# Kernel optimization log

Measured on AMD Instinct MI355X. Metric: run time of the kernel, lower is better.

## Reference

```python
import jax, jax.numpy as jnp
import numpy as np

NUM_GROUPS = 128
GROUP_SIZE = 1024
N_POINTS = 262144


def setup_inputs() -> dict:
    key = jax.random.key(0)
    k1, k2, k3, k4 = jax.random.split(key, 4)
    point_cloud = jax.random.normal(k1, (1, 3, N_POINTS), dtype=jnp.float32)
    # pointwise-MLP feature extractor params (3 -> 64 -> 128 -> 1024)
    w1 = jax.random.normal(k2, (3, 64), dtype=jnp.float32) * 0.1
    w2 = jax.random.normal(k3, (64, 128), dtype=jnp.float32) * 0.1
    w3 = jax.random.normal(k4, (128, 1024), dtype=jnp.float32) * 0.03
    return {"point_cloud": point_cloud, "w1": w1, "w2": w2, "w3": w3}


def _fps(points, num_groups):
    # points: [N, 3]. Seed = point farthest from the centroid (as in source),
    # then iterative farthest-point sampling. The source recomputes distances
    # to every sampled point each step; keeping a running min-distance is
    # mathematically identical.
    centroid = points.mean(axis=0, keepdims=True)
    d0 = jnp.linalg.norm(points - centroid, axis=1)  # [N]
    first = jnp.argmax(d0)
    min_dist = jnp.linalg.norm(points - points[first], axis=1)  # [N]

    def step(min_dist, _):
        nxt = jnp.argmax(min_dist)
        d = jnp.linalg.norm(points - points[nxt], axis=1)
        return jnp.minimum(min_dist, d), nxt

    _, idx_rest = jax.lax.scan(step, min_dist, None, length=num_groups - 1)
    return jnp.concatenate([first[None], idx_rest])  # [G]


def reference(point_cloud, w1, w2, w3):
    pc = point_cloud[0].T  # [N, 3]  (squeeze(0).permute(1,0))
    fps_idx = _fps(pc, NUM_GROUPS)
    sampled = pc[fps_idx]  # [G, 3]
    # Brute-force KNN (sklearn kneighbors equivalent): squared dists [G, N]
    d2 = (jnp.sum(sampled * sampled, axis=1, keepdims=True)
          - 2.0 * (sampled @ pc.T)
          + jnp.sum(pc * pc, axis=1)[None, :])
    _, knn_idx = jax.lax.top_k(-d2, GROUP_SIZE)  # [G, K] nearest indices
    groups = pc[knn_idx]  # [G, K, 3] irregular gather
    # feature_: per-point MLP + max-pool over the K points of each patch.
    # (Pointwise op => batching all G groups at once equals the source's
    # pairwise batched calls.)
    h = jax.nn.relu(groups @ w1)       # [G, K, 64]
    h = jax.nn.relu(h @ w2)            # [G, K, 128]
    h = h @ w3                         # [G, K, 1024]
    patch_features = h.max(axis=1)     # [G, 1024]
    return patch_features, sampled
```

## Files before the change

### kernel.cpp

```cpp
#include <hip/hip_runtime.h>

#define N_PTS 262144
#define NG 128
#define GS 1024
#define FPS_B 16

typedef __attribute__((ext_vector_type(8))) short short8;
typedef __attribute__((ext_vector_type(8))) __bf16 bf16x8;
typedef __attribute__((ext_vector_type(4))) float f32x4;
typedef unsigned long long ull;

__device__ __forceinline__ unsigned short f2bf(float f) {
  unsigned u = __float_as_uint(f);
  unsigned r = u + 0x7FFFu + ((u >> 16) & 1u);
  return (unsigned short)(r >> 16);
}

__device__ __forceinline__ f32x4 mfma16(short8 a, short8 b, f32x4 c) {
  return __builtin_amdgcn_mfma_f32_16x16x32_bf16(
      __builtin_bit_cast(bf16x8, a), __builtin_bit_cast(bf16x8, b), c, 0, 0, 0);
}

__device__ __forceinline__ ull shfl_xor_u64(ull v, int m) {
  unsigned lo = __shfl_xor((unsigned)v, m);
  unsigned hi = __shfl_xor((unsigned)(v >> 32), m);
  return ((ull)hi << 32) | lo;
}

__device__ __forceinline__ void st64(ull* p, ull v) {
  __hip_atomic_store(p, v, __ATOMIC_RELAXED, __HIP_MEMORY_SCOPE_AGENT);
}
__device__ __forceinline__ ull ld64(const ull* p) {
  return __hip_atomic_load(p, __ATOMIC_RELAXED, __HIP_MEMORY_SCOPE_AGENT);
}

__device__ __forceinline__ unsigned ordenc(float f) {
  unsigned u = __float_as_uint(f);
  return (u >> 31) ? ~u : (u | 0x80000000u);
}

__device__ __forceinline__ unsigned knn_key(float x, float y, float z, float pp,
                                            float sx, float sy, float sz, float s2) {
  float dot = __fmaf_rn(sx, x, __fmaf_rn(sy, y, __fmul_rn(sz, z)));
  float d2 = __fadd_rn(__fsub_rn(s2, __fadd_rn(dot, dot)), pp);
  return ordenc(d2);
}

__device__ __forceinline__ void select_bucket(const unsigned* hist, int nbins,
                                              unsigned krem, unsigned* sres, int lane) {
  const int per = nbins >> 6;
  unsigned local = 0;
  for (int j = 0; j < per; ++j) local += hist[lane * per + j];
  unsigned inc = local;
  for (int off = 1; off < 64; off <<= 1) {
    unsigned v = __shfl_up(inc, off);
    if (lane >= off) inc += v;
  }
  unsigned exc = inc - local;
  if (exc < krem && krem <= inc) {
    unsigned c = exc;
    for (int j = 0; j < per; ++j) {
      unsigned h = hist[lane * per + j];
      if (c + h >= krem) { sres[0] = (unsigned)(lane * per + j); sres[1] = c; break; }
      c += h;
    }
  }
}

__global__ void __launch_bounds__(1024) fps_knn_kernel(const float* __restrict__ pc,
    const float* __restrict__ w2, const float* __restrict__ w3,
    unsigned short* __restrict__ w2t, unsigned short* __restrict__ w3t,
    float* __restrict__ sampled_out, int* __restrict__ knn,
    unsigned* __restrict__ cnts, ull* __restrict__ kslots, ull* __restrict__ mb,
    ull* __restrict__ cslots) {
  __shared__ __align__(16) char sbuf[90112];
  __shared__ unsigned sres[2];
  __shared__ unsigned scnt[6];
  __shared__ float mbx[3];
  __shared__ float rs[3][16];
  __shared__ ull wkeyL[16];
  __shared__ float bc[3];
  const int tid = threadIdx.x;
  const int lane = tid & 63, wv = tid >> 6;

  if (blockIdx.x >= FPS_B) {
    const int g = blockIdx.x - FPS_B;
    {
      int i3 = g * 1024 + tid;
      { int n = i3 >> 7, k = i3 & 127; w3t[i3] = f2bf(w3[k * 1024 + n]); }
      if (g < 8) { int i2 = g * 1024 + tid; int n = i2 >> 6, k = i2 & 63; w2t[i2] = f2bf(w2[k * 128 + n]); }
    }
    unsigned* hist = (unsigned*)sbuf;
    unsigned* candk = (unsigned*)(sbuf + 8192);
    unsigned* candi = (unsigned*)(sbuf + 40960);
    unsigned* candk2 = (unsigned*)(sbuf + 73728);
    unsigned* candi2 = (unsigned*)(sbuf + 81920);
    for (int i = tid; i < 2048; i += 1024) hist[i] = 0u;
    if (tid < 6) scnt[tid] = 0u;
    if (tid < 3) {
      ull v;
      for (;;) {
        v = ld64(&mb[g * 16 + tid]);
        if ((unsigned)v == (unsigned)(g + 1)) break;
        __builtin_amdgcn_s_sleep(64);
      }
      mbx[tid] = __uint_as_float((unsigned)(v >> 32));
    }
    __syncthreads();
    const float sx = mbx[0], sy = mbx[1], sz = mbx[2];
    const float s2 = __fadd_rn(__fadd_rn(__fmul_rn(sx, sx), __fmul_rn(sy, sy)),
                               __fmul_rn(sz, sz));
    const f32x4* xs4 = (const f32x4*)pc;
    const f32x4* ys4 = (const f32x4*)(pc + N_PTS);
    const f32x4* zs4 = (const f32x4*)(pc + 2 * N_PTS);
    for (int it = 0; it < 4; ++it) {
      int i4 = it * 1024 + tid;
      f32x4 xv = xs4[i4], yv = ys4[i4], zv = zs4[i4];
#pragma unroll
      for (int u = 0; u < 4; ++u) {
        float pp = __fadd_rn(__fadd_rn(__fmul_rn(xv[u], xv[u]), __fmul_rn(yv[u], yv[u])),
                             __fmul_rn(zv[u], zv[u]));
        unsigned k = knn_key(xv[u], yv[u], zv[u], pp, sx, sy, sz, s2);
        atomicAdd(&hist[k >> 21], 1u);
      }
    }
    __syncthreads();
    if (tid < 64) select_bucket(hist, 2048, 160u, sres, lane);
    __syncthreads();
    const unsigned Tp = (sres[0] >= 2047u) ? 0xFFFFFFFFu : ((sres[0] + 1u) << 21);
    __syncthreads();
    for (int it = 0; it < 64; ++it) {
      int i4 = it * 1024 + tid;
      f32x4 xv = xs4[i4], yv = ys4[i4], zv = zs4[i4];
#pragma unroll
      for (int u = 0; u < 4; ++u) {
        float pp = __fadd_rn(__fadd_rn(__fmul_rn(xv[u], xv[u]), __fmul_rn(yv[u], yv[u])),
                             __fmul_rn(zv[u], zv[u]));
        unsigned k = knn_key(xv[u], yv[u], zv[u], pp, sx, sy, sz, s2);
        if (k < Tp) {
          unsigned e = atomicAdd(&scnt[0], 1u);
          if (e < 8192u) { candk[e] = k; candi[e] = (unsigned)(i4 * 4 + u); }
        }
      }
    }
    __syncthreads();
    const int m = (int)min(scnt[0], 8192u);
    for (int i = tid; i < 2048; i += 1024) hist[i] = 0u;
    __syncthreads();
    for (int j = tid; j < m; j += 1024) atomicAdd(&hist[candk[j] >> 21], 1u);
    __syncthreads();
    if (tid < 64) select_bucket(hist, 2048, GS, sres, lane);
    __syncthreads();
    const unsigned bA = sres[0];
    unsigned krem = GS - sres[1];
    __syncthreads();
    for (int j = tid; j < m; j += 1024) {
      unsigned k = candk[j], b = k >> 21;
      if (b < bA) {
        unsigned pos = atomicAdd(&scnt[1], 1u);
        knn[g * GS + (int)pos] = (int)candi[j];
      } else if (b == bA) {
        unsigned e = atomicAdd(&scnt[2], 1u);
        if (e < 2048u) { candk2[e] = k; candi2[e] = candi[j]; }
      }
    }
    __syncthreads();
    const int m2 = (int)min(scnt[2], 2048u);
    const int base1 = (int)scnt[1];
    for (int i = tid; i < 2048; i += 1024) hist[i] = 0u;
    __syncthreads();
    for (int j = tid; j < m2; j += 1024) atomicAdd(&hist[(candk2[j] >> 10) & 2047u], 1u);
    __syncthreads();
    if (tid < 64) select_bucket(hist, 2048, krem, sres, lane);
    __syncthreads();
    const unsigned bB = sres[0];
    krem -= sres[1];
    __syncthreads();
    if (tid < 1024) hist[tid] = 0u;
    __syncthreads();
    for (int j = tid; j < m2; j += 1024)
      if (((candk2[j] >> 10) & 2047u) == bB) atomicAdd(&hist[candk2[j] & 1023u], 1u);
    __syncthreads();
    if (tid < 64) select_bucket(hist, 1024, krem, sres, lane);
    __syncthreads();
    const unsigned bC = sres[0];
    krem -= sres[1];
    const unsigned T = (bA << 21) | (bB << 10) | bC;
    __syncthreads();
    for (int j = tid; j < m2; j += 1024) {
      unsigned k = candk2[j];
      if (k < T) {
        unsigned pos = atomicAdd(&scnt[3], 1u);
        knn[g * GS + base1 + (int)pos] = (int)candi2[j];
      } else if (k == T) {
        unsigned e = atomicAdd(&scnt[4], 1u);
        if (e < 2048u) hist[e] = candi2[j];
      }
    }
    __syncthreads();
    if (tid < 64) {
      const int tc = (int)min(scnt[4], 2048u);
      const int base2 = base1 + (int)scnt[3];
      for (int j = 0; j < (int)krem; ++j) {
        int best = 0x7FFFFFFF;
        for (int q = lane; q < tc; q += 64) best = min(best, (int)hist[q]);
        for (int mm = 32; mm; mm >>= 1) best = min(best, __shfl_xor(best, mm));
        for (int q = lane; q < tc; q += 64)
          if ((int)hist[q] == best) hist[q] = 0x7FFFFFFFu;
        if (lane == 0) knn[g * GS + base2 + j] = best;
      }
    }
    return;
  }

  const int p = blockIdx.x;
  const int gt = p * 1024 + tid;
  const float* xs = pc;
  const float* ys = pc + N_PTS;
  const float* zs = pc + 2 * N_PTS;
  float x[16], y[16], z[16], md[16];
  float sx = 0.f, sy = 0.f, sz = 0.f;
#pragma unroll
  for (int j = 0; j < 16; ++j) {
    int i = gt + j * 16384;
    x[j] = xs[i]; y[j] = ys[i]; z[j] = zs[i];
    sx += x[j]; sy += y[j]; sz += z[j];
  }
#pragma unroll
  for (int m = 32; m; m >>= 1) {
    sx += __shfl_xor(sx, m); sy += __shfl_xor(sy, m); sz += __shfl_xor(sz, m);
  }
  if (lane == 0) { rs[0][wv] = sx; rs[1][wv] = sy; rs[2][wv] = sz; }
  __syncthreads();
  if (tid == 0) {
    float ax = 0.f, ay = 0.f, az = 0.f;
    for (int w = 0; w < 16; ++w) { ax += rs[0][w]; ay += rs[1][w]; az += rs[2][w]; }
    st64(&cslots[0 + p], (ull)__float_as_uint(ax));
    st64(&cslots[16 + p], (ull)__float_as_uint(ay));
    st64(&cslots[32 + p], (ull)__float_as_uint(az));
    __hip_atomic_fetch_add(&cnts[4], 1u, __ATOMIC_RELEASE, __HIP_MEMORY_SCOPE_AGENT);
  }
  if (wv == 0) {
    while (__hip_atomic_load(&cnts[4], __ATOMIC_RELAXED, __HIP_MEMORY_SCOPE_AGENT) < 16u)
      __builtin_amdgcn_s_sleep(1);
    (void)__hip_atomic_load(&cnts[4], __ATOMIC_ACQUIRE, __HIP_MEMORY_SCOPE_AGENT);
    float f = 0.f;
    if (lane < 48) f = __uint_as_float((unsigned)ld64(&cslots[lane]));
    float s = 0.f;
    for (int q = 0; q < 16; ++q) s += __shfl(f, (lane & 48) + q);
    if (lane == 0)  bc[0] = s * (1.f / N_PTS);
    if (lane == 16) bc[1] = s * (1.f / N_PTS);
    if (lane == 32) bc[2] = s * (1.f / N_PTS);
  }
  __syncthreads();
  ull lkey = 0ull;
  {
    float cx = bc[0], cy = bc[1], cz = bc[2];
#pragma unroll
    for (int j = 0; j < 16; ++j) {
      float dx = x[j] - cx, dy = y[j] - cy, dz = z[j] - cz;
      float d = __fmaf_rn(dx, dx, __fmaf_rn(dy, dy, dz * dz));
      md[j] = d;
      unsigned fb = __float_as_uint(d);
      ull k = ((ull)fb << 18) | (ull)(0x3FFFFu ^ (unsigned)(gt + j * 16384));
      if (k > lkey) lkey = k;
    }
  }
  for (int sel = 0; sel < NG; ++sel) {
    const ull seq = (ull)(sel + 1);
    ull rk = lkey;
#pragma unroll
    for (int m = 32; m; m >>= 1) {
      ull o = shfl_xor_u64(rk, m);
      if (o > rk) rk = o;
    }
    if (lane == 0) wkeyL[wv] = rk;
    __syncthreads();
    if (wv == 0) {
      const int pb = (sel & 1) * 16;
      ull bk = (lane < 16) ? wkeyL[lane] : 0ull;
#pragma unroll
      for (int m = 8; m; m >>= 1) {
        ull o = shfl_xor_u64(bk, m);
        if (o > bk) bk = o;
      }
      if (lane == 0) st64(&kslots[pb + p], (seq << 50) | bk);
      ull v = 0ull; float c = 0.f;
      bool got = (lane >= 48);
      for (;;) {
        if (!got) {
          v = ld64(&kslots[pb + (lane & 15)]);
          if ((v >> 50) == seq) {
            got = true;
            unsigned idx = 0x3FFFFu ^ (unsigned)(v & 0x3FFFFull);
            c = pc[(lane >> 4) * N_PTS + idx];
          }
        }
        if (__all((int)got)) break;
      }
      ull gk = v;
      int ws_ = lane & 15;
#pragma unroll
      for (int m = 8; m; m >>= 1) {
        ull o = shfl_xor_u64(gk, m);
        int ow = __shfl_xor(ws_, m);
        if (o > gk) { gk = o; ws_ = ow; }
      }
      if (lane < 48 && (lane & 15) == ws_) {
        bc[lane >> 4] = c;
        if (p == 0) {
          sampled_out[sel * 3 + (lane >> 4)] = c;
          st64(&mb[sel * 16 + (lane >> 4)], ((ull)__float_as_uint(c) << 32) | seq);
        }
      }
    }
    __syncthreads();
    {
      float wx = bc[0], wy = bc[1], wz = bc[2];
      ull nk = 0ull;
#pragma unroll
      for (int j = 0; j < 16; ++j) {
        float dx = x[j] - wx, dy = y[j] - wy, dz = z[j] - wz;
        float d = __fmaf_rn(dx, dx, __fmaf_rn(dy, dy, dz * dz));
        float m = (sel == 0) ? d : fminf(md[j], d);
        md[j] = m;
        unsigned fb = __float_as_uint(m);
        ull k = ((ull)fb << 18) | (ull)(0x3FFFFu ^ (unsigned)(gt + j * 16384));
        if (k > nk) nk = k;
      }
      lkey = nk;
    }
  }
}

__global__ void __launch_bounds__(256, 2) mlp_kernel(const float* __restrict__ pc,
    const int* __restrict__ knn, const float* __restrict__ w1,
    const unsigned short* __restrict__ w2t, const unsigned short* __restrict__ w3t,
    unsigned* __restrict__ gout) {
  const int blk = blockIdx.x, g = blk >> 2, split = blk & 3;
  const int tid = threadIdx.x, lane = tid & 63, wv = tid >> 6;
  __shared__ unsigned gmax[1024];
  __shared__ __align__(16) short h1[128 * 72];
  __shared__ __align__(16) short h2[128 * 136];
  __shared__ float cxs[128], cys[128], czs[128];
  for (int i = tid; i < 1024; i += 256) gmax[i] = 0u;
  const float* xs = pc;
  const float* ys = pc + N_PTS;
  const float* zs = pc + 2 * N_PTS;
  const int ch = tid & 63;
  const int pgrp = tid >> 6;
  const float w10 = w1[ch], w11 = w1[64 + ch], w12 = w1[128 + ch];
  const int r0 = (lane >> 4) * 4;
  const int cB = lane & 15;
  const int kB = (lane >> 4) * 8;
  for (int tile = 0; tile < 2; ++tile) {
    __syncthreads();
    if (tid < 128) {
      int i = knn[g * 1024 + split * 256 + tile * 128 + tid];
      cxs[tid] = xs[i]; cys[tid] = ys[i]; czs[tid] = zs[i];
    }
    __syncthreads();
    for (int q = 0; q < 32; ++q) {
      int p = pgrp * 32 + q;
      float v = fmaxf(__fmaf_rn(cxs[p], w10, __fmaf_rn(cys[p], w11, czs[p] * w12)), 0.f);
      h1[p * 72 + ch] = (short)f2bf(v);
    }
    __syncthreads();
    {
      short8 a[2][2];
#pragma unroll
      for (int mt = 0; mt < 2; ++mt)
#pragma unroll
        for (int ks = 0; ks < 2; ++ks)
          a[mt][ks] = *(const short8*)&h1[((2 * wv + mt) * 16 + cB) * 72 + kB + ks * 32];
#pragma unroll
      for (int n0 = 0; n0 < 8; ++n0) {
        short8 bb[2];
#pragma unroll
        for (int ks = 0; ks < 2; ++ks)
          bb[ks] = *(const short8*)&w2t[(n0 * 16 + cB) * 64 + kB + ks * 32];
#pragma unroll
        for (int mt = 0; mt < 2; ++mt) {
          f32x4 acc = {0.f, 0.f, 0.f, 0.f};
          acc = mfma16(a[mt][0], bb[0], acc);
          acc = mfma16(a[mt][1], bb[1], acc);
          int rr = (2 * wv + mt) * 16 + r0;
#pragma unroll
          for (int r = 0; r < 4; ++r)
            h2[(rr + r) * 136 + n0 * 16 + cB] = (short)f2bf(fmaxf(acc[r], 0.f));
        }
      }
    }
    __syncthreads();
    {
      short8 a2[2][4];
#pragma unroll
      for (int mt = 0; mt < 2; ++mt)
#pragma unroll
        for (int ks = 0; ks < 4; ++ks)
          a2[mt][ks] = *(const short8*)&h2[((2 * wv + mt) * 16 + cB) * 136 + kB + ks * 32];
      for (int n0 = 0; n0 < 64; ++n0) {
        short8 b3[4];
#pragma unroll
        for (int ks = 0; ks < 4; ++ks)
          b3[ks] = *(const short8*)&w3t[(n0 * 16 + cB) * 128 + kB + ks * 32];
        f32x4 acc0 = {0.f, 0.f, 0.f, 0.f}, acc1 = {0.f, 0.f, 0.f, 0.f};
#pragma unroll
        for (int ks = 0; ks < 4; ++ks) acc0 = mfma16(a2[0][ks], b3[ks], acc0);
#pragma unroll
        for (int ks = 0; ks < 4; ++ks) acc1 = mfma16(a2[1][ks], b3[ks], acc1);
        float mv = fmaxf(fmaxf(fmaxf(acc0[0], acc0[1]), fmaxf(acc0[2], acc0[3])),
                         fmaxf(fmaxf(acc1[0], acc1[1]), fmaxf(acc1[2], acc1[3])));
        mv = fmaxf(mv, __shfl_xor(mv, 16));
        mv = fmaxf(mv, __shfl_xor(mv, 32));
        if (lane < 16) atomicMax(&gmax[n0 * 16 + lane], ordenc(mv));
      }
    }
  }
  __syncthreads();
  for (int i = tid; i < 1024; i += 256)
    gout[(g * 4 + split) * 1024 + i] = gmax[i];
}

__global__ void __launch_bounds__(256) combine_kernel(const unsigned* __restrict__ gm,
                                                      float* __restrict__ out) {
  int c = blockIdx.x * 256 + threadIdx.x;
  int g = c >> 10, chn = c & 1023;
  unsigned m = 0u;
#pragma unroll
  for (int s = 0; s < 4; ++s) {
    unsigned v = gm[(g * 4 + s) * 1024 + chn];
    if (v > m) m = v;
  }
  out[c] = (m >> 31) ? __uint_as_float(m ^ 0x80000000u) : __uint_as_float(~m);
}

extern "C" void kernel_launch(void* const* d_in, const int* in_sizes, int n_in,
                              void* d_out, int out_size, void* d_ws, size_t ws_size,
                              hipStream_t stream) {
  (void)in_sizes; (void)n_in; (void)out_size; (void)ws_size;
  const float* pc = (const float*)d_in[0];
  const float* w1 = (const float*)d_in[1];
  const float* w2 = (const float*)d_in[2];
  const float* w3 = (const float*)d_in[3];
  float* out = (float*)d_out;
  char* ws = (char*)d_ws;

  unsigned* cnts = (unsigned*)(ws + 0);
  ull* kslots = (ull*)(ws + 128);
  ull* cslots = (ull*)(ws + 1024);
  ull* mb = (ull*)(ws + 2048);
  unsigned short* w2t = (unsigned short*)(ws + 24576);
  unsigned short* w3t = (unsigned short*)(ws + 24576 + 16384);
  int* knn = (int*)(ws + 24576 + 16384 + 262144);
  unsigned* gout = (unsigned*)(ws + 24576 + 16384 + 262144 + 524288);
  float* sampled = out + 131072;

  hipMemsetAsync(ws, 0, 20480, stream);
  fps_knn_kernel<<<FPS_B + NG, 1024, 0, stream>>>(pc, w2, w3, w2t, w3t, sampled,
                                                  knn, cnts, kslots, mb, cslots);
  mlp_kernel<<<NG * 4, 256, 0, stream>>>(pc, knn, w1, w2t, w3t, gout);
  combine_kernel<<<512, 256, 0, stream>>>(gout, out);
}
```

Baseline: 576.1 us.

## Fuse KNN selection and pointwise MLP max-pool into the FPS kernel

Each KNN block now keeps its selected neighbor indices in shared memory and runs the MLP and max-pool itself, writing final features straight to the output. This removes the separate MLP and combine launches and the global knn and partial-max buffers. A new global counter makes each block wait until all weight-transpose prep is done before using the bf16 weights. The cost is that each group's MLP runs on a single 1024-thread block, 128 blocks in total, instead of being split across 512 smaller blocks, which lowers parallelism for the MLP phase.

Result: slower. 926.6 us (+60.8%).

```diff
diff --git a/kernel.cpp b/kernel.cpp
--- a/kernel.cpp
+++ b/kernel.cpp
@@ -67,13 +67,15 @@
   }
 }
 
-__global__ void __launch_bounds__(1024) fps_knn_kernel(const float* __restrict__ pc,
-    const float* __restrict__ w2, const float* __restrict__ w3,
-    unsigned short* __restrict__ w2t, unsigned short* __restrict__ w3t,
-    float* __restrict__ sampled_out, int* __restrict__ knn,
-    unsigned* __restrict__ cnts, ull* __restrict__ kslots, ull* __restrict__ mb,
-    ull* __restrict__ cslots) {
-  __shared__ __align__(16) char sbuf[90112];
+__global__ void __launch_bounds__(1024) fused_kernel(const float* __restrict__ pc,
+    const float* __restrict__ w1, const float* __restrict__ w2,
+    const float* __restrict__ w3, unsigned short* __restrict__ w2t,
+    unsigned short* __restrict__ w3t, float* __restrict__ out,
+    unsigned* __restrict__ cnts, unsigned* __restrict__ prepcnt,
+    ull* __restrict__ kslots, ull* __restrict__ mb, ull* __restrict__ cslots) {
+  __shared__ __align__(16) char sbuf[109568];
+  __shared__ int idxL[1024];
+  __shared__ unsigned gmax[1024];
   __shared__ unsigned sres[2];
   __shared__ unsigned scnt[6];
   __shared__ float mbx[3];
@@ -82,6 +84,9 @@
   __shared__ float bc[3];
   const int tid = threadIdx.x;
   const int lane = tid & 63, wv = tid >> 6;
+  const float* xs = pc;
+  const float* ys = pc + N_PTS;
+  const float* zs = pc + 2 * N_PTS;
 
   if (blockIdx.x >= FPS_B) {
     const int g = blockIdx.x - FPS_B;
@@ -90,12 +95,16 @@
       { int n = i3 >> 7, k = i3 & 127; w3t[i3] = f2bf(w3[k * 1024 + n]); }
       if (g < 8) { int i2 = g * 1024 + tid; int n = i2 >> 6, k = i2 & 63; w2t[i2] = f2bf(w2[k * 128 + n]); }
     }
+    __syncthreads();
+    if (tid == 0)
+      __hip_atomic_fetch_add(prepcnt, 1u, __ATOMIC_RELEASE, __HIP_MEMORY_SCOPE_AGENT);
     unsigned* hist = (unsigned*)sbuf;
     unsigned* candk = (unsigned*)(sbuf + 8192);
     unsigned* candi = (unsigned*)(sbuf + 40960);
     unsigned* candk2 = (unsigned*)(sbuf + 73728);
     unsigned* candi2 = (unsigned*)(sbuf + 81920);
     for (int i = tid; i < 2048; i += 1024) hist[i] = 0u;
+    gmax[tid] = 0u;
     if (tid < 6) scnt[tid] = 0u;
     if (tid < 3) {
       ull v;
@@ -158,7 +167,7 @@
       unsigned k = candk[j], b = k >> 21;
       if (b < bA) {
         unsigned pos = atomicAdd(&scnt[1], 1u);
-        knn[g * GS + (int)pos] = (int)candi[j];
+        idxL[pos] = (int)candi[j];
       } else if (b == bA) {
         unsigned e = atomicAdd(&scnt[2], 1u);
         if (e < 2048u) { candk2[e] = k; candi2[e] = candi[j]; }
@@ -191,7 +200,7 @@
       unsigned k = candk2[j];
       if (k < T) {
         unsigned pos = atomicAdd(&scnt[3], 1u);
-        knn[g * GS + base1 + (int)pos] = (int)candi2[j];
+        idxL[base1 + (int)pos] = (int)candi2[j];
       } else if (k == T) {
         unsigned e = atomicAdd(&scnt[4], 1u);
         if (e < 2048u) hist[e] = candi2[j];
@@ -207,17 +216,96 @@
         for (int mm = 32; mm; mm >>= 1) best = min(best, __shfl_xor(best, mm));
         for (int q = lane; q < tc; q += 64)
           if ((int)hist[q] == best) hist[q] = 0x7FFFFFFFu;
-        if (lane == 0) knn[g * GS + base2 + j] = best;
-      }
+        if (lane == 0) idxL[base2 + j] = best;
+      }
+    }
+    if (tid == 0) {
+      while (__hip_atomic_load(prepcnt, __ATOMIC_RELAXED, __HIP_MEMORY_SCOPE_AGENT) < 128u)
+        __builtin_amdgcn_s_sleep(8);
+      (void)__hip_atomic_load(prepcnt, __ATOMIC_ACQUIRE, __HIP_MEMORY_SCOPE_AGENT);
+    }
+    __syncthreads();
+    const int half = tid >> 9, htid = tid & 511;
+    const int hlane = htid & 63, rb = htid >> 6;
+    short* h1 = (short*)(sbuf + half * 54784);
+    short* h2 = (short*)(sbuf + half * 54784 + 18432);
+    float* cxs = (float*)(sbuf + half * 54784 + 53248);
+    float* cys = (float*)(sbuf + half * 54784 + 53760);
+    float* czs = (float*)(sbuf + half * 54784 + 54272);
+    const int ch = htid & 63;
+    const float w10 = w1[ch], w11 = w1[64 + ch], w12 = w1[128 + ch];
+    const int cB = hlane & 15, kB = (hlane >> 4) * 8, r0 = (hlane >> 4) * 4;
+    for (int spi = 0; spi < 2; ++spi) {
+      const int sp = half * 2 + spi;
+      for (int tile = 0; tile < 2; ++tile) {
+        __syncthreads();
+        if (htid < 128) {
+          int i = idxL[sp * 256 + tile * 128 + htid];
+          cxs[htid] = xs[i]; cys[htid] = ys[i]; czs[htid] = zs[i];
+        }
+        __syncthreads();
+        {
+          const int pg = htid >> 6;
+          for (int q = 0; q < 16; ++q) {
+            int p = pg * 16 + q;
+            float v = fmaxf(__fmaf_rn(cxs[p], w10, __fmaf_rn(cys[p], w11, czs[p] * w12)), 0.f);
+            h1[p * 72 + ch] = (short)f2bf(v);
+          }
+        }
+        __syncthreads();
+        {
+          short8 a[2];
+#pragma unroll
+          for (int ks = 0; ks < 2; ++ks)
+            a[ks] = *(const short8*)&h1[(rb * 16 + cB) * 72 + kB + ks * 32];
+#pragma unroll
+          for (int n0 = 0; n0 < 8; ++n0) {
+            short8 bb[2];
+#pragma unroll
+            for (int ks = 0; ks < 2; ++ks)
+              bb[ks] = *(const short8*)&w2t[(n0 * 16 + cB) * 64 + kB + ks * 32];
+            f32x4 acc = {0.f, 0.f, 0.f, 0.f};
+            acc = mfma16(a[0], bb[0], acc);
+            acc = mfma16(a[1], bb[1], acc);
+#pragma unroll
+            for (int r = 0; r < 4; ++r)
+              h2[(rb * 16 + r0 + r) * 136 + n0 * 16 + cB] = (short)f2bf(fmaxf(acc[r], 0.f));
+          }
+        }
+        __syncthreads();
+        {
+          short8 a2[4];
+#pragma unroll
+          for (int ks = 0; ks < 4; ++ks)
+            a2[ks] = *(const short8*)&h2[(rb * 16 + cB) * 136 + kB + ks * 32];
+          for (int n0 = 0; n0 < 64; ++n0) {
+            short8 b3[4];
+#pragma unroll
+            for (int ks = 0; ks < 4; ++ks)
+              b3[ks] = *(const short8*)&w3t[(n0 * 16 + cB) * 128 + kB + ks * 32];
+            f32x4 acc = {0.f, 0.f, 0.f, 0.f};
+#pragma unroll
+            for (int ks = 0; ks < 4; ++ks) acc = mfma16(a2[ks], b3[ks], acc);
+            float mv = fmaxf(fmaxf(acc[0], acc[1]), fmaxf(acc[2], acc[3]));
+            mv = fmaxf(mv, __shfl_xor(mv, 16));
+            mv = fmaxf(mv, __shfl_xor(mv, 32));
+            if (hlane < 16) atomicMax(&gmax[n0 * 16 + hlane], ordenc(mv));
+          }
+        }
+      }
+    }
+    __syncthreads();
+    {
+      unsigned mm = gmax[tid];
+      out[g * 1024 + tid] = (mm >> 31) ? __uint_as_float(mm ^ 0x80000000u)
+                                       : __uint_as_float(~mm);
     }
     return;
   }
 
   const int p = blockIdx.x;
   const int gt = p * 1024 + tid;
-  const float* xs = pc;
-  const float* ys = pc + N_PTS;
-  const float* zs = pc + 2 * N_PTS;
+  float* sampled_out = out + 131072;
   float x[16], y[16], z[16], md[16];
   float sx = 0.f, sy = 0.f, sz = 0.f;
 #pragma unroll
@@ -333,108 +421,6 @@
   }
 }
 
-__global__ void __launch_bounds__(256, 2) mlp_kernel(const float* __restrict__ pc,
-    const int* __restrict__ knn, const float* __restrict__ w1,
-    const unsigned short* __restrict__ w2t, const unsigned short* __restrict__ w3t,
-    unsigned* __restrict__ gout) {
-  const int blk = blockIdx.x, g = blk >> 2, split = blk & 3;
-  const int tid = threadIdx.x, lane = tid & 63, wv = tid >> 6;
-  __shared__ unsigned gmax[1024];
-  __shared__ __align__(16) short h1[128 * 72];
-  __shared__ __align__(16) short h2[128 * 136];
-  __shared__ float cxs[128], cys[128], czs[128];
-  for (int i = tid; i < 1024; i += 256) gmax[i] = 0u;
-  const float* xs = pc;
-  const float* ys = pc + N_PTS;
-  const float* zs = pc + 2 * N_PTS;
-  const int ch = tid & 63;
-  const int pgrp = tid >> 6;
-  const float w10 = w1[ch], w11 = w1[64 + ch], w12 = w1[128 + ch];
-  const int r0 = (lane >> 4) * 4;
-  const int cB = lane & 15;
-  const int kB = (lane >> 4) * 8;
-  for (int tile = 0; tile < 2; ++tile) {
-    __syncthreads();
-    if (tid < 128) {
-      int i = knn[g * 1024 + split * 256 + tile * 128 + tid];
-      cxs[tid] = xs[i]; cys[tid] = ys[i]; czs[tid] = zs[i];
-    }
-    __syncthreads();
-    for (int q = 0; q < 32; ++q) {
-      int p = pgrp * 32 + q;
-      float v = fmaxf(__fmaf_rn(cxs[p], w10, __fmaf_rn(cys[p], w11, czs[p] * w12)), 0.f);
-      h1[p * 72 + ch] = (short)f2bf(v);
-    }
-    __syncthreads();
-    {
-      short8 a[2][2];
-#pragma unroll
-      for (int mt = 0; mt < 2; ++mt)
-#pragma unroll
-        for (int ks = 0; ks < 2; ++ks)
-          a[mt][ks] = *(const short8*)&h1[((2 * wv + mt) * 16 + cB) * 72 + kB + ks * 32];
-#pragma unroll
-      for (int n0 = 0; n0 < 8; ++n0) {
-        short8 bb[2];
-#pragma unroll
-        for (int ks = 0; ks < 2; ++ks)
-          bb[ks] = *(const short8*)&w2t[(n0 * 16 + cB) * 64 + kB + ks * 32];
-#pragma unroll
-        for (int mt = 0; mt < 2; ++mt) {
-          f32x4 acc = {0.f, 0.f, 0.f, 0.f};
-          acc = mfma16(a[mt][0], bb[0], acc);
-          acc = mfma16(a[mt][1], bb[1], acc);
-          int rr = (2 * wv + mt) * 16 + r0;
-#pragma unroll
-          for (int r = 0; r < 4; ++r)
-            h2[(rr + r) * 136 + n0 * 16 + cB] = (short)f2bf(fmaxf(acc[r], 0.f));
-        }
-      }
-    }
-    __syncthreads();
-    {
-      short8 a2[2][4];
-#pragma unroll
-      for (int mt = 0; mt < 2; ++mt)
-#pragma unroll
-        for (int ks = 0; ks < 4; ++ks)
-          a2[mt][ks] = *(const short8*)&h2[((2 * wv + mt) * 16 + cB) * 136 + kB + ks * 32];
-      for (int n0 = 0; n0 < 64; ++n0) {
-        short8 b3[4];
-#pragma unroll
-        for (int ks = 0; ks < 4; ++ks)
-          b3[ks] = *(const short8*)&w3t[(n0 * 16 + cB) * 128 + kB + ks * 32];
-        f32x4 acc0 = {0.f, 0.f, 0.f, 0.f}, acc1 = {0.f, 0.f, 0.f, 0.f};
-#pragma unroll
-        for (int ks = 0; ks < 4; ++ks) acc0 = mfma16(a2[0][ks], b3[ks], acc0);
-#pragma unroll
-        for (int ks = 0; ks < 4; ++ks) acc1 = mfma16(a2[1][ks], b3[ks], acc1);
-        float mv = fmaxf(fmaxf(fmaxf(acc0[0], acc0[1]), fmaxf(acc0[2], acc0[3])),
-                         fmaxf(fmaxf(acc1[0], acc1[1]), fmaxf(acc1[2], acc1[3])));
-        mv = fmaxf(mv, __shfl_xor(mv, 16));
-        mv = fmaxf(mv, __shfl_xor(mv, 32));
-        if (lane < 16) atomicMax(&gmax[n0 * 16 + lane], ordenc(mv));
-      }
-    }
-  }
-  __syncthreads();
-  for (int i = tid; i < 1024; i += 256)
-    gout[(g * 4 + split) * 1024 + i] = gmax[i];
-}
-
-__global__ void __launch_bounds__(256) combine_kernel(const unsigned* __restrict__ gm,
-                                                      float* __restrict__ out) {
-  int c = blockIdx.x * 256 + threadIdx.x;
-  int g = c >> 10, chn = c & 1023;
-  unsigned m = 0u;
-#pragma unroll
-  for (int s = 0; s < 4; ++s) {
-    unsigned v = gm[(g * 4 + s) * 1024 + chn];
-    if (v > m) m = v;
-  }
-  out[c] = (m >> 31) ? __uint_as_float(m ^ 0x80000000u) : __uint_as_float(~m);
-}
-
 extern "C" void kernel_launch(void* const* d_in, const int* in_sizes, int n_in,
                               void* d_out, int out_size, void* d_ws, size_t ws_size,
                               hipStream_t stream) {
@@ -447,18 +433,14 @@
   char* ws = (char*)d_ws;
 
   unsigned* cnts = (unsigned*)(ws + 0);
+  unsigned* prepcnt = (unsigned*)(ws + 64);
   ull* kslots = (ull*)(ws + 128);
   ull* cslots = (ull*)(ws + 1024);
   ull* mb = (ull*)(ws + 2048);
   unsigned short* w2t = (unsigned short*)(ws + 24576);
   unsigned short* w3t = (unsigned short*)(ws + 24576 + 16384);
-  int* knn = (int*)(ws + 24576 + 16384 + 262144);
-  unsigned* gout = (unsigned*)(ws + 24576 + 16384 + 262144 + 524288);
-  float* sampled = out + 131072;
 
   hipMemsetAsync(ws, 0, 20480, stream);
-  fps_knn_kernel<<<FPS_B + NG, 1024, 0, stream>>>(pc, w2, w3, w2t, w3t, sampled,
-                                                  knn, cnts, kslots, mb, cslots);
-  mlp_kernel<<<NG * 4, 256, 0, stream>>>(pc, knn, w1, w2t, w3t, gout);
-  combine_kernel<<<512, 256, 0, stream>>>(gout, out);
-}
+  fused_kernel<<<FPS_B + NG, 1024, 0, stream>>>(pc, w1, w2, w3, w2t, w3t, out,
+                                                cnts, prepcnt, kslots, mb, cslots);
+}
```

## Fuse combine into MLP kernel via last-block counter and preload all points

Applied to the files above, without the earlier changes.

Removes the separate combine kernel launch. Each of the four split blocks per group writes its partial max, then increments a per-group counter, and the last block to arrive reduces the four partials and writes the final output. It also gathers all 256 points in one load before the tile loop instead of one load per tile, which removes one barrier and the serialized gather. The cost is extra atomics and fences, plus a tail reduction done by only the last block of each group.

New measurement: 584.0 us. Within noise of the previous version (+1.4%).

```diff
diff --git a/kernel.cpp b/kernel.cpp
--- a/kernel.cpp
+++ b/kernel.cpp
@@ -336,13 +336,15 @@
 __global__ void __launch_bounds__(256, 2) mlp_kernel(const float* __restrict__ pc,
     const int* __restrict__ knn, const float* __restrict__ w1,
     const unsigned short* __restrict__ w2t, const unsigned short* __restrict__ w3t,
-    unsigned* __restrict__ gout) {
+    unsigned* __restrict__ gout, unsigned* __restrict__ gcnt,
+    float* __restrict__ out) {
   const int blk = blockIdx.x, g = blk >> 2, split = blk & 3;
   const int tid = threadIdx.x, lane = tid & 63, wv = tid >> 6;
   __shared__ unsigned gmax[1024];
   __shared__ __align__(16) short h1[128 * 72];
   __shared__ __align__(16) short h2[128 * 136];
-  __shared__ float cxs[128], cys[128], czs[128];
+  __shared__ float cxs[256], cys[256], czs[256];
+  __shared__ unsigned lastS;
   for (int i = tid; i < 1024; i += 256) gmax[i] = 0u;
   const float* xs = pc;
   const float* ys = pc + N_PTS;
@@ -353,16 +355,17 @@
   const int r0 = (lane >> 4) * 4;
   const int cB = lane & 15;
   const int kB = (lane >> 4) * 8;
+  {
+    int i = knn[g * 1024 + split * 256 + tid];
+    cxs[tid] = xs[i]; cys[tid] = ys[i]; czs[tid] = zs[i];
+  }
   for (int tile = 0; tile < 2; ++tile) {
-    __syncthreads();
-    if (tid < 128) {
-      int i = knn[g * 1024 + split * 256 + tile * 128 + tid];
-      cxs[tid] = xs[i]; cys[tid] = ys[i]; czs[tid] = zs[i];
-    }
     __syncthreads();
     for (int q = 0; q < 32; ++q) {
       int p = pgrp * 32 + q;
-      float v = fmaxf(__fmaf_rn(cxs[p], w10, __fmaf_rn(cys[p], w11, czs[p] * w12)), 0.f);
+      float v = fmaxf(__fmaf_rn(cxs[tile * 128 + p], w10,
+                                __fmaf_rn(cys[tile * 128 + p], w11,
+                                          czs[tile * 128 + p] * w12)), 0.f);
       h1[p * 72 + ch] = (short)f2bf(v);
     }
     __syncthreads();
@@ -419,20 +422,26 @@
   }
   __syncthreads();
   for (int i = tid; i < 1024; i += 256)
-    gout[(g * 4 + split) * 1024 + i] = gmax[i];
-}
-
-__global__ void __launch_bounds__(256) combine_kernel(const unsigned* __restrict__ gm,
-                                                      float* __restrict__ out) {
-  int c = blockIdx.x * 256 + threadIdx.x;
-  int g = c >> 10, chn = c & 1023;
-  unsigned m = 0u;
-#pragma unroll
-  for (int s = 0; s < 4; ++s) {
-    unsigned v = gm[(g * 4 + s) * 1024 + chn];
-    if (v > m) m = v;
-  }
-  out[c] = (m >> 31) ? __uint_as_float(m ^ 0x80000000u) : __uint_as_float(~m);
+    __hip_atomic_store(&gout[(g * 4 + split) * 1024 + i], gmax[i],
+                       __ATOMIC_RELAXED, __HIP_MEMORY_SCOPE_AGENT);
+  __syncthreads();
+  if (tid == 0)
+    lastS = __hip_atomic_fetch_add(&gcnt[g], 1u, __ATOMIC_ACQ_REL,
+                                   __HIP_MEMORY_SCOPE_AGENT);
+  __syncthreads();
+  if (lastS == 3u) {
+    for (int i = tid; i < 1024; i += 256) {
+      unsigned mm = 0u;
+#pragma unroll
+      for (int s = 0; s < 4; ++s) {
+        unsigned v = __hip_atomic_load(&gout[(g * 4 + s) * 1024 + i],
+                                       __ATOMIC_RELAXED, __HIP_MEMORY_SCOPE_AGENT);
+        if (v > mm) mm = v;
+      }
+      out[g * 1024 + i] = (mm >> 31) ? __uint_as_float(mm ^ 0x80000000u)
+                                     : __uint_as_float(~mm);
+    }
+  }
 }
 
 extern "C" void kernel_launch(void* const* d_in, const int* in_sizes, int n_in,
@@ -450,6 +459,7 @@
   ull* kslots = (ull*)(ws + 128);
   ull* cslots = (ull*)(ws + 1024);
   ull* mb = (ull*)(ws + 2048);
+  unsigned* gcnt = (unsigned*)(ws + 18432);
   unsigned short* w2t = (unsigned short*)(ws + 24576);
   unsigned short* w3t = (unsigned short*)(ws + 24576 + 16384);
   int* knn = (int*)(ws + 24576 + 16384 + 262144);
@@ -459,6 +469,5 @@
   hipMemsetAsync(ws, 0, 20480, stream);
   fps_knn_kernel<<<FPS_B + NG, 1024, 0, stream>>>(pc, w2, w3, w2t, w3t, sampled,
                                                   knn, cnts, kslots, mb, cslots);
-  mlp_kernel<<<NG * 4, 256, 0, stream>>>(pc, knn, w1, w2t, w3t, gout);
-  combine_kernel<<<512, 256, 0, stream>>>(gout, out);
-}
+  mlp_kernel<<<NG * 4, 256, 0, stream>>>(pc, knn, w1, w2t, w3t, gout, gcnt, out);
+}
```
